# Kernel tuning notes

Hardware: AMD Instinct MI355X
Metric: run time of the kernel (lower is better)

The kernel has to match this reference:

```python
import jax, jax.numpy as jnp
import numpy as np

B, N, C, H = 4, 2048, 1024, 16
HD = C // H            # head dim = 64
HALF = HD // 2         # complex pairs per head = 32
VR = 32.0              # virtual_resolution
THETA = 10.0           # rope_theta


def _init_freqs():
    # mirrors init_3d_freqs_unified + per-axis replication with small noise
    rng = np.random.default_rng(0)
    idx = np.arange(HALF, dtype=np.float32)
    base = 1.0 / THETA ** (2.0 * idx / HD)                 # [HALF]
    angles = rng.uniform(0, 2 * np.pi, size=(H, 1)).astype(np.float32)
    per_head = base[None, :] * np.cos(angles)              # [H, HALF]
    freqs = np.repeat(per_head[None], 3, axis=0)           # [3, H, HALF]
    freqs = freqs + rng.normal(0, 0.01, freqs.shape).astype(np.float32)
    return jnp.asarray(freqs.reshape(3, H * HALF), dtype=jnp.float32)


def setup_inputs() -> dict:
    key = jax.random.key(0)
    ks = jax.random.split(key, 7)
    x = jax.random.normal(ks[0], (B, N, C), dtype=jnp.float32)
    t_x = jax.random.uniform(ks[1], (N,), dtype=jnp.float32)
    t_y = jax.random.uniform(ks[2], (N,), dtype=jnp.float32)
    t_z = jax.random.uniform(ks[3], (N,), dtype=jnp.float32)
    w_qkv = jax.random.normal(ks[4], (3 * C, C), dtype=jnp.float32) * (C ** -0.5)
    w_proj = jax.random.normal(ks[5], (C, C), dtype=jnp.float32) * (C ** -0.5)
    b_proj = jnp.zeros((C,), dtype=jnp.float32)
    freqs = _init_freqs()
    return {"x": x, "t_x": t_x, "t_y": t_y, "t_z": t_z,
            "w_qkv": w_qkv, "w_proj": w_proj, "b_proj": b_proj, "freqs": freqs}


def _normalize(t):
    # normalize_point_coords_3d with 'virtual_resolution'
    return (t - t.min()) / (t.max() - t.min() + 1e-8) * VR


def reference(x, t_x, t_y, t_z, w_qkv, w_proj, b_proj, freqs):
    # QKV projection (no bias)
    qkv = (x @ w_qkv.T).reshape(B, N, 3, H, HD).transpose(2, 0, 3, 1, 4)  # [3,B,H,N,HD]
    q, k, v = qkv[0], qkv[1], qkv[2]

    # mixed 3D RoPE angles: outer(t_axis, freqs[axis]) summed over axes
    tx, ty, tz = _normalize(t_x), _normalize(t_y), _normalize(t_z)
    ang = (tx[:, None] * freqs[0] + ty[:, None] * freqs[1] + tz[:, None] * freqs[2])  # [N, H*HALF]
    ang = ang.reshape(N, H, HALF).transpose(1, 0, 2)       # [H, N, HALF]
    cos, sin = jnp.cos(ang), jnp.sin(ang)

    def rotate(t):
        # complex multiply (a+ib)*(cos+isin) on even/odd pairs of last dim
        tr = t.reshape(B, H, N, HALF, 2)
        a, b = tr[..., 0], tr[..., 1]
        ra = a * cos - b * sin
        rb = a * sin + b * cos
        return jnp.stack([ra, rb], axis=-1).reshape(B, H, N, HD)

    q = rotate(q)
    k = rotate(k)

    scale = HD ** -0.5
    attn = jax.nn.softmax(jnp.einsum('bhnd,bhmd->bhnm', q * scale, k), axis=-1)
    out = jnp.einsum('bhnm,bhmd->bhnd', attn, v).transpose(0, 2, 1, 3).reshape(B, N, C)
    return out @ w_proj.T + b_proj
```

## Files before the change

kernel.cpp:

```cpp
#include <hip/hip_runtime.h>
#include <math.h>

#define BB 4
#define NN 2048
#define CC 1024
#define HH 16
#define HD 64
#define HALF 32
#define MM (BB*NN)
#define K3 (3*CC)
#define NF (HH*HALF)
#define NT (NN/64)

typedef __attribute__((ext_vector_type(8))) short bf16x8;
typedef __attribute__((ext_vector_type(4))) float f32x4;
typedef __attribute__((ext_vector_type(16))) float f32x16;
typedef __attribute__((ext_vector_type(4))) unsigned short u16x4;
typedef __attribute__((ext_vector_type(8))) unsigned short u16x8;
typedef __attribute__((ext_vector_type(4))) unsigned int u32x4;

#if __has_builtin(__builtin_amdgcn_exp2f)
#define EXP2(x) __builtin_amdgcn_exp2f(x)
#else
#define EXP2(x) exp2f(x)
#endif
#define AS1 __attribute__((address_space(1)))
#define AS3 __attribute__((address_space(3)))

__device__ __forceinline__ unsigned short f2bf(float f) {
    unsigned int u = __float_as_uint(f);
    unsigned int r = (u + 0x7FFFu + ((u >> 16) & 1u)) >> 16;
    return (unsigned short)r;
}

__global__ __launch_bounds__(256) void tnorm_kernel(const float* t_x, const float* t_y,
                                                    const float* t_z, float* tnorm) {
    int a = blockIdx.x;
    const float* t = (a == 0) ? t_x : ((a == 1) ? t_y : t_z);
    __shared__ float smn[256], smx[256];
    float mn = 1e30f, mx = -1e30f;
    for (int i = threadIdx.x; i < NN; i += 256) {
        float v = t[i];
        mn = fminf(mn, v);
        mx = fmaxf(mx, v);
    }
    smn[threadIdx.x] = mn; smx[threadIdx.x] = mx;
    __syncthreads();
    for (int s = 128; s > 0; s >>= 1) {
        if (threadIdx.x < s) {
            smn[threadIdx.x] = fminf(smn[threadIdx.x], smn[threadIdx.x + s]);
            smx[threadIdx.x] = fmaxf(smx[threadIdx.x], smx[threadIdx.x + s]);
        }
        __syncthreads();
    }
    float lo = smn[0];
    float sc = 32.0f / (smx[0] - lo + 1e-8f);
    for (int i = threadIdx.x; i < NN; i += 256)
        tnorm[a * NN + i] = (t[i] - lo) * sc;
}

__global__ __launch_bounds__(512) void angle_kernel(const float* freqs, const float* tnorm,
                                                    float* cosT, float* sinT) {
    int n = blockIdx.x;
    int hf = threadIdx.x;
    float ang = tnorm[n] * freqs[hf]
              + tnorm[NN + n] * freqs[NF + hf]
              + tnorm[2 * NN + n] * freqs[2 * NF + hf];
    cosT[(size_t)n * NF + hf] = cosf(ang);
    sinT[(size_t)n * NF + hf] = sinf(ang);
}

__global__ __launch_bounds__(256) void cvt_kernel(const float* __restrict__ src,
                                                  unsigned short* __restrict__ dst, int n) {
    int i = (blockIdx.x * 256 + threadIdx.x) * 8;
    if (i < n) {
        float4 a = *(const float4*)(src + i);
        float4 b = *(const float4*)(src + i + 4);
        u16x8 o;
        o[0] = f2bf(a.x); o[1] = f2bf(a.y); o[2] = f2bf(a.z); o[3] = f2bf(a.w);
        o[4] = f2bf(b.x); o[5] = f2bf(b.y); o[6] = f2bf(b.z); o[7] = f2bf(b.w);
        *(u16x8*)(dst + i) = o;
    }
}

__global__ __launch_bounds__(256) void qkv_gemm_kernel(const unsigned short* __restrict__ A,
                                                       const unsigned short* __restrict__ Bw,
                                                       const float* __restrict__ cosT,
                                                       const float* __restrict__ sinT,
                                                       unsigned short* __restrict__ qb,
                                                       unsigned short* __restrict__ kb,
                                                       unsigned short* __restrict__ vbT) {
    __shared__ unsigned short Asl[128 * 64];
    __shared__ unsigned short Bsl[128 * 64];
    const int tid = threadIdx.x;
    const int wv = tid >> 6, l = tid & 63;
    const int wm = wv >> 1, wn = wv & 1;
    const int lg = l >> 4, l15 = l & 15;
    const int m0 = blockIdx.x * 128, n0 = blockIdx.y * 128;

    f32x4 acc[4][4];
#pragma unroll
    for (int i = 0; i < 4; i++)
#pragma unroll
        for (int j = 0; j < 4; j++) acc[i][j] = f32x4{0.f, 0.f, 0.f, 0.f};

    for (int kt = 0; kt < CC; kt += 64) {
        __syncthreads();
#pragma unroll
        for (int i = 0; i < 4; i++) {
            int c = (wv * 4 + i) * 64 + l;
            int r = c >> 3, kc = c & 7;
            int sc = kt + ((kc ^ (r & 7)) * 8);
            __builtin_amdgcn_global_load_lds(
                (AS1 void*)(A + (size_t)(m0 + r) * CC + sc),
                (AS3 void*)(&Asl[(wv * 4 + i) * 512]), 16, 0, 0);
            __builtin_amdgcn_global_load_lds(
                (AS1 void*)(Bw + (size_t)(n0 + r) * CC + sc),
                (AS3 void*)(&Bsl[(wv * 4 + i) * 512]), 16, 0, 0);
        }
        __syncthreads();
#pragma unroll
        for (int kc = 0; kc < 2; kc++) {
            bf16x8 af[4], bfr[4];
#pragma unroll
            for (int mi = 0; mi < 4; mi++) {
                int r = wm * 64 + mi * 16 + l15;
                af[mi] = *(const bf16x8*)(&Asl[r * 64 + (((kc * 4 + lg) ^ (r & 7)) * 8)]);
            }
#pragma unroll
            for (int nj = 0; nj < 4; nj++) {
                int r = wn * 64 + nj * 16 + l15;
                bfr[nj] = *(const bf16x8*)(&Bsl[r * 64 + (((kc * 4 + lg) ^ (r & 7)) * 8)]);
            }
#pragma unroll
            for (int mi = 0; mi < 4; mi++)
#pragma unroll
                for (int nj = 0; nj < 4; nj++)
                    acc[mi][nj] = __builtin_amdgcn_mfma_f32_16x16x32_bf16(af[mi], bfr[nj], acc[mi][nj], 0, 0, 0);
        }
    }
    const int b_ = m0 >> 11;
    const int nrow0 = (m0 & (NN - 1));
#pragma unroll
    for (int nj = 0; nj < 4; nj++) {
        int oc = n0 + wn * 64 + nj * 16 + l15;
        int s = oc >> 10;
        int rr = oc & 1023;
        int h = rr >> 6;
        int d = rr & 63;
        int f = d >> 1;
#pragma unroll
        for (int mi = 0; mi < 4; mi++) {
            f32x4 v = acc[mi][nj];
            if (s == 2) {
                u16x4 vv;
#pragma unroll
                for (int reg = 0; reg < 4; reg++) vv[reg] = f2bf(v[reg]);
                int nb = nrow0 + wm * 64 + mi * 16 + lg * 4;
                *(u16x4*)(vbT + ((size_t)((b_ * HH + h) * HD + d)) * NN + nb) = vv;
            } else {
#pragma unroll
                for (int reg = 0; reg < 4; reg++) {
                    int m = m0 + wm * 64 + mi * 16 + lg * 4 + reg;
                    int n = m & (NN - 1);
                    float val = v[reg];
                    float partner = __shfl_xor(val, 1);
                    size_t base = (((size_t)(b_ * HH + h)) * NN + n) * HD + d;
                    float cs = cosT[(size_t)n * NF + h * HALF + f];
                    float sn = sinT[(size_t)n * NF + h * HALF + f];
                    float res = ((d & 1) == 0) ? (val * cs - partner * sn)
                                               : (val * cs + partner * sn);
                    if (s == 0) res *= 0.18033688011112043f;
                    (s == 0 ? qb : kb)[base] = f2bf(res);
                }
            }
        }
    }
}

template<int BUF>
__device__ __forceinline__ void attn_iter(
    unsigned short* LB, bool do_stage, int wv, int l31,
    const unsigned short*& kn0, const unsigned short*& kn1,
    const unsigned short*& vn0, const unsigned short*& vn1,
    const int (&so)[4], const bf16x8 (&qfA)[4], const bf16x8 (&qfB)[4],
    const f32x16& Z, const bf16x8& ones,
    f32x16& OA0, f32x16& OA1, f32x16& OB0, f32x16& OB1,
    f32x16& SsA, f32x16& SsB) {
    if (do_stage) {
        const int nb = (BUF ^ 1) * 4096;
        __builtin_amdgcn_global_load_lds((AS1 void*)kn0, (AS3 void*)(&LB[nb + (wv * 2 + 0) * 512]), 16, 0, 0);
        __builtin_amdgcn_global_load_lds((AS1 void*)kn1, (AS3 void*)(&LB[nb + (wv * 2 + 1) * 512]), 16, 0, 0);
        __builtin_amdgcn_global_load_lds((AS1 void*)vn0, (AS3 void*)(&LB[8192 + nb + (wv * 2 + 0) * 512]), 16, 0, 0);
        __builtin_amdgcn_global_load_lds((AS1 void*)vn1, (AS3 void*)(&LB[8192 + nb + (wv * 2 + 1) * 512]), 16, 0, 0);
        kn0 += 4096; kn1 += 4096; vn0 += 64; vn1 += 64;
    }
    f32x16 sA0, sA1, sB0, sB1;
    __builtin_amdgcn_s_setprio(1);
    {
        bf16x8 a0 = *(const bf16x8*)(LB + BUF * 4096 + l31 * 64 + so[0]);
        bf16x8 a1 = *(const bf16x8*)(LB + BUF * 4096 + (32 + l31) * 64 + so[0]);
        sA0 = __builtin_amdgcn_mfma_f32_32x32x16_bf16(a0, qfA[0], Z, 0, 0, 0);
        sA1 = __builtin_amdgcn_mfma_f32_32x32x16_bf16(a1, qfA[0], Z, 0, 0, 0);
        sB0 = __builtin_amdgcn_mfma_f32_32x32x16_bf16(a0, qfB[0], Z, 0, 0, 0);
        sB1 = __builtin_amdgcn_mfma_f32_32x32x16_bf16(a1, qfB[0], Z, 0, 0, 0);
    }
#pragma unroll
    for (int dc = 1; dc < 4; dc++) {
        bf16x8 a0 = *(const bf16x8*)(LB + BUF * 4096 + l31 * 64 + so[dc]);
        bf16x8 a1 = *(const bf16x8*)(LB + BUF * 4096 + (32 + l31) * 64 + so[dc]);
        sA0 = __builtin_amdgcn_mfma_f32_32x32x16_bf16(a0, qfA[dc], sA0, 0, 0, 0);
        sA1 = __builtin_amdgcn_mfma_f32_32x32x16_bf16(a1, qfA[dc], sA1, 0, 0, 0);
        sB0 = __builtin_amdgcn_mfma_f32_32x32x16_bf16(a0, qfB[dc], sB0, 0, 0, 0);
        sB1 = __builtin_amdgcn_mfma_f32_32x32x16_bf16(a1, qfB[dc], sB1, 0, 0, 0);
    }
    __builtin_amdgcn_s_setprio(0);
#pragma unroll
    for (int r = 0; r < 16; r++) {
        sA0[r] = EXP2(sA0[r]); sA1[r] = EXP2(sA1[r]);
        sB0[r] = EXP2(sB0[r]); sB1[r] = EXP2(sB1[r]);
    }
#pragma unroll
    for (int r = 0; r < 8; r++) {
        unsigned u0, u1, u2, u3;
        asm("v_cvt_pk_bf16_f32 %0, %1, %2" : "=v"(u0) : "v"(sA0[2 * r]), "v"(sA0[2 * r + 1]));
        asm("v_cvt_pk_bf16_f32 %0, %1, %2" : "=v"(u1) : "v"(sA1[2 * r]), "v"(sA1[2 * r + 1]));
        asm("v_cvt_pk_bf16_f32 %0, %1, %2" : "=v"(u2) : "v"(sB0[2 * r]), "v"(sB0[2 * r + 1]));
        asm("v_cvt_pk_bf16_f32 %0, %1, %2" : "=v"(u3) : "v"(sB1[2 * r]), "v"(sB1[2 * r + 1]));
        sA0[2 * r] = __uint_as_float(u0);
        sA1[2 * r] = __uint_as_float(u1);
        sB0[2 * r] = __uint_as_float(u2);
        sB1[2 * r] = __uint_as_float(u3);
    }
    __builtin_amdgcn_s_setprio(1);
#pragma unroll
    for (int kc = 0; kc < 4; kc++) {
        const int bs = (kc & 1) * 8;
        bf16x8 pfA, pfB;
        {
            float e0 = (kc < 2) ? sA0[bs + 0] : sA1[bs + 0];
            float e4 = (kc < 2) ? sA0[bs + 4] : sA1[bs + 4];
            float e2 = (kc < 2) ? sA0[bs + 2] : sA1[bs + 2];
            float e6 = (kc < 2) ? sA0[bs + 6] : sA1[bs + 6];
            auto uA = __builtin_amdgcn_permlane32_swap(__float_as_uint(e0), __float_as_uint(e4), false, false);
            auto uB = __builtin_amdgcn_permlane32_swap(__float_as_uint(e2), __float_as_uint(e6), false, false);
            u32x4 t; t.x = uA[0]; t.y = uB[0]; t.z = uA[1]; t.w = uB[1];
            pfA = __builtin_bit_cast(bf16x8, t);
        }
        {
            float e0 = (kc < 2) ? sB0[bs + 0] : sB1[bs + 0];
            float e4 = (kc < 2) ? sB0[bs + 4] : sB1[bs + 4];
            float e2 = (kc < 2) ? sB0[bs + 2] : sB1[bs + 2];
            float e6 = (kc < 2) ? sB0[bs + 6] : sB1[bs + 6];
            auto uA = __builtin_amdgcn_permlane32_swap(__float_as_uint(e0), __float_as_uint(e4), false, false);
            auto uB = __builtin_amdgcn_permlane32_swap(__float_as_uint(e2), __float_as_uint(e6), false, false);
            u32x4 t; t.x = uA[0]; t.y = uB[0]; t.z = uA[1]; t.w = uB[1];
            pfB = __builtin_bit_cast(bf16x8, t);
        }
        bf16x8 va  = *(const bf16x8*)(LB + 8192 + BUF * 4096 + l31 * 64 + so[kc]);
        bf16x8 vb2 = *(const bf16x8*)(LB + 8192 + BUF * 4096 + (32 + l31) * 64 + so[kc]);
        OA0 = __builtin_amdgcn_mfma_f32_32x32x16_bf16(va,  pfA, OA0, 0, 0, 0);
        OA1 = __builtin_amdgcn_mfma_f32_32x32x16_bf16(vb2, pfA, OA1, 0, 0, 0);
        OB0 = __builtin_amdgcn_mfma_f32_32x32x16_bf16(va,  pfB, OB0, 0, 0, 0);
        OB1 = __builtin_amdgcn_mfma_f32_32x32x16_bf16(vb2, pfB, OB1, 0, 0, 0);
        SsA = __builtin_amdgcn_mfma_f32_32x32x16_bf16(ones, pfA, SsA, 0, 0, 0);
        SsB = __builtin_amdgcn_mfma_f32_32x32x16_bf16(ones, pfB, SsB, 0, 0, 0);
    }
    __builtin_amdgcn_s_setprio(0);
    __syncthreads();
}

__global__ __launch_bounds__(256, 2) void attn_mfma_kernel(const unsigned short* __restrict__ qbp,
                                                           const unsigned short* __restrict__ kbp,
                                                           const unsigned short* __restrict__ vtp,
                                                           unsigned short* __restrict__ aout) {
    __shared__ unsigned short LB[4 * 4096];
    const int tid = threadIdx.x;
    const int wv = tid >> 6;
    const int l = tid & 63;
    const int l31 = l & 31, hi = l >> 5;

    const int wg = blockIdx.x;
    const int Lidx = (wg & 7) * 64 + (wg >> 3);
    const int bh = Lidx >> 3;
    const int q0 = (Lidx & 7) * 256;

    const unsigned short* qp = qbp + (size_t)bh * (NN * HD);
    const unsigned short* kp = kbp + (size_t)bh * (NN * HD);
    const unsigned short* vp = vtp + (size_t)bh * (NN * HD);

    const int r0 = (wv * 2 + 0) * 8 + (l >> 3);
    const int r1 = (wv * 2 + 1) * 8 + (l >> 3);
    const int c0 = ((l & 7) ^ (r0 & 7)) * 8;
    const int c1 = ((l & 7) ^ (r1 & 7)) * 8;
    const unsigned short* kn0 = kp + r0 * HD + c0;
    const unsigned short* kn1 = kp + r1 * HD + c1;
    const unsigned short* vn0 = vp + (size_t)r0 * NN + c0;
    const unsigned short* vn1 = vp + (size_t)r1 * NN + c1;

    __builtin_amdgcn_global_load_lds((AS1 void*)kn0, (AS3 void*)(&LB[(wv * 2 + 0) * 512]), 16, 0, 0);
    __builtin_amdgcn_global_load_lds((AS1 void*)kn1, (AS3 void*)(&LB[(wv * 2 + 1) * 512]), 16, 0, 0);
    __builtin_amdgcn_global_load_lds((AS1 void*)vn0, (AS3 void*)(&LB[8192 + (wv * 2 + 0) * 512]), 16, 0, 0);
    __builtin_amdgcn_global_load_lds((AS1 void*)vn1, (AS3 void*)(&LB[8192 + (wv * 2 + 1) * 512]), 16, 0, 0);
    kn0 += 4096; kn1 += 4096; vn0 += 64; vn1 += 64;

    const unsigned short* qr = qp + (size_t)(q0 + wv * 64 + l31) * HD;
    bf16x8 qfA[4], qfB[4];
#pragma unroll
    for (int dc = 0; dc < 4; dc++) {
        qfA[dc] = *(const bf16x8*)(qr + dc * 16 + hi * 8);
        qfB[dc] = *(const bf16x8*)(qr + 32 * HD + dc * 16 + hi * 8);
    }

    int so[4];
#pragma unroll
    for (int i = 0; i < 4; i++) so[i] = ((2 * i + hi) ^ (l31 & 7)) * 8;

    f32x16 Z;
#pragma unroll
    for (int r = 0; r < 16; r++) Z[r] = 0.0f;
    f32x16 OA0 = Z, OA1 = Z, OB0 = Z, OB1 = Z, SsA = Z, SsB = Z;
    bf16x8 ones;
#pragma unroll
    for (int j = 0; j < 8; j++) ones[j] = (short)0x3F80;

    __syncthreads();

    for (int ktb = 0; ktb < NT; ktb += 2) {
        attn_iter<0>(LB, true, wv, l31, kn0, kn1, vn0, vn1, so, qfA, qfB,
                     Z, ones, OA0, OA1, OB0, OB1, SsA, SsB);
        attn_iter<1>(LB, ktb + 2 < NT, wv, l31, kn0, kn1, vn0, vn1, so, qfA, qfB,
                     Z, ones, OA0, OA1, OB0, OB1, SsA, SsB);
    }

    const int b_ = bh >> 4, hh = bh & 15;
    const float invA = 1.0f / SsA[0], invB = 1.0f / SsB[0];
    const size_t mrowA = (size_t)(b_ * NN + q0 + wv * 64 + l31) * CC + hh * HD;
    const size_t mrowB = mrowA + (size_t)32 * CC;
#pragma unroll
    for (int rq = 0; rq < 4; rq++) {
        u16x4 a0, a1, b0, b1;
#pragma unroll
        for (int j = 0; j < 4; j++) {
            a0[j] = f2bf(OA0[rq * 4 + j] * invA);
            a1[j] = f2bf(OA1[rq * 4 + j] * invA);
            b0[j] = f2bf(OB0[rq * 4 + j] * invB);
            b1[j] = f2bf(OB1[rq * 4 + j] * invB);
        }
        *(u16x4*)(aout + mrowA + rq * 8 + hi * 4) = a0;
        *(u16x4*)(aout + mrowA + 32 + rq * 8 + hi * 4) = a1;
        *(u16x4*)(aout + mrowB + rq * 8 + hi * 4) = b0;
        *(u16x4*)(aout + mrowB + 32 + rq * 8 + hi * 4) = b1;
    }
}

__global__ __launch_bounds__(256) void proj_gemm_kernel(const unsigned short* __restrict__ A,
                                                        const unsigned short* __restrict__ Bw,
                                                        const float* __restrict__ bp,
                                                        float* __restrict__ out) {
    __shared__ unsigned short Asl[128 * 64];
    __shared__ unsigned short Bsl[128 * 64];
    const int tid = threadIdx.x;
    const int wv = tid >> 6, l = tid & 63;
    const int wm = wv >> 1, wn = wv & 1;
    const int lg = l >> 4, l15 = l & 15;
    const int m0 = blockIdx.x * 128, n0 = blockIdx.y * 128;

    f32x4 acc[4][4];
#pragma unroll
    for (int i = 0; i < 4; i++)
#pragma unroll
        for (int j = 0; j < 4; j++) acc[i][j] = f32x4{0.f, 0.f, 0.f, 0.f};

    for (int kt = 0; kt < CC; kt += 64) {
        __syncthreads();
#pragma unroll
        for (int i = 0; i < 4; i++) {
            int c = (wv * 4 + i) * 64 + l;
            int r = c >> 3, kc = c & 7;
            int sc = kt + ((kc ^ (r & 7)) * 8);
            __builtin_amdgcn_global_load_lds(
                (AS1 void*)(A + (size_t)(m0 + r) * CC + sc),
                (AS3 void*)(&Asl[(wv * 4 + i) * 512]), 16, 0, 0);
            __builtin_amdgcn_global_load_lds(
                (AS1 void*)(Bw + (size_t)(n0 + r) * CC + sc),
                (AS3 void*)(&Bsl[(wv * 4 + i) * 512]), 16, 0, 0);
        }
        __syncthreads();
#pragma unroll
        for (int kc = 0; kc < 2; kc++) {
            bf16x8 af[4], bfr[4];
#pragma unroll
            for (int mi = 0; mi < 4; mi++) {
                int r = wm * 64 + mi * 16 + l15;
                af[mi] = *(const bf16x8*)(&Asl[r * 64 + (((kc * 4 + lg) ^ (r & 7)) * 8)]);
            }
#pragma unroll
            for (int nj = 0; nj < 4; nj++) {
                int r = wn * 64 + nj * 16 + l15;
                bfr[nj] = *(const bf16x8*)(&Bsl[r * 64 + (((kc * 4 + lg) ^ (r & 7)) * 8)]);
            }
#pragma unroll
            for (int mi = 0; mi < 4; mi++)
#pragma unroll
                for (int nj = 0; nj < 4; nj++)
                    acc[mi][nj] = __builtin_amdgcn_mfma_f32_16x16x32_bf16(af[mi], bfr[nj], acc[mi][nj], 0, 0, 0);
        }
    }
    float bias[4];
#pragma unroll
    for (int nj = 0; nj < 4; nj++) bias[nj] = bp[n0 + wn * 64 + nj * 16 + l15];
#pragma unroll
    for (int mi = 0; mi < 4; mi++)
#pragma unroll
        for (int nj = 0; nj < 4; nj++) {
            int oc = n0 + wn * 64 + nj * 16 + l15;
#pragma unroll
            for (int reg = 0; reg < 4; reg++) {
                int m = m0 + wm * 64 + mi * 16 + lg * 4 + reg;
                out[(size_t)m * CC + oc] = acc[mi][nj][reg] + bias[nj];
            }
        }
}

extern "C" void kernel_launch(void* const* d_in, const int* in_sizes, int n_in,
                              void* d_out, int out_size, void* d_ws, size_t ws_size,
                              hipStream_t stream) {
    const float* x      = (const float*)d_in[0];
    const float* t_x    = (const float*)d_in[1];
    const float* t_y    = (const float*)d_in[2];
    const float* t_z    = (const float*)d_in[3];
    const float* w_qkv  = (const float*)d_in[4];
    const float* w_proj = (const float*)d_in[5];
    const float* b_proj = (const float*)d_in[6];
    const float* freqs  = (const float*)d_in[7];
    float* out = (float*)d_out;

    unsigned short* xb     = (unsigned short*)d_ws;
    unsigned short* wqkvb  = xb + (size_t)MM * CC;
    unsigned short* wprojb = wqkvb + (size_t)K3 * CC;
    unsigned short* qbuf   = wprojb + (size_t)CC * CC;
    unsigned short* kbuf   = qbuf + (size_t)BB * HH * NN * HD;
    unsigned short* vbT    = kbuf + (size_t)BB * HH * NN * HD;
    unsigned short* attnb  = vbT + (size_t)BB * HH * NN * HD;
    float* cosT  = (float*)(attnb + (size_t)MM * CC);
    float* sinT  = cosT + (size_t)NN * NF;
    float* tnorm = sinT + (size_t)NN * NF;

    tnorm_kernel<<<3, 256, 0, stream>>>(t_x, t_y, t_z, tnorm);
    angle_kernel<<<NN, 512, 0, stream>>>(freqs, tnorm, cosT, sinT);
    cvt_kernel<<<(MM * CC) / 2048, 256, 0, stream>>>(x, xb, MM * CC);
    cvt_kernel<<<(K3 * CC) / 2048, 256, 0, stream>>>(w_qkv, wqkvb, K3 * CC);
    cvt_kernel<<<(CC * CC) / 2048, 256, 0, stream>>>(w_proj, wprojb, CC * CC);
    qkv_gemm_kernel<<<dim3(MM / 128, K3 / 128), 256, 0, stream>>>(xb, wqkvb, cosT, sinT,
                                                                  qbuf, kbuf, vbT);
    attn_mfma_kernel<<<512, 256, 0, stream>>>(qbuf, kbuf, vbT, attnb);
    proj_gemm_kernel<<<dim3(MM / 128, CC / 128), 256, 0, stream>>>(attnb, wprojb, b_proj, out);
}
```

Measured before the change: 210.4 us.

## Switch attention to single-wave workgroups with 32-key tiles and no barriers

Restructures the attention kernel so each 64-thread workgroup holds one wave that owns 64 query rows, launching 2048 blocks instead of 512 four-wave blocks. K and V tiles shrink to 32 keys and are double-buffered in an 8192-element LDS buffer, with a new rotated-XOR swizzle for the staged layout. Block-wide __syncthreads is replaced by explicit s_waitcnt on vmcnt and lgkmcnt, so only the wave's own ordering is enforced. The intent is to remove barrier stalls and give the scheduler more independent waves, at the cost of each wave loading its own K/V with no sharing across waves and of smaller MFMA batches per iteration.

```diff
diff --git a/kernel.cpp b/kernel.cpp
--- a/kernel.cpp
+++ b/kernel.cpp
@@ -10,7 +10,8 @@
 #define MM (BB*NN)
 #define K3 (3*CC)
 #define NF (HH*HALF)
-#define NT (NN/64)
+#define TK 32
+#define NT2 (NN/TK)
 
 typedef __attribute__((ext_vector_type(8))) short bf16x8;
 typedef __attribute__((ext_vector_type(4))) float f32x4;
@@ -179,142 +180,143 @@
 }
 
 template<int BUF>
-__device__ __forceinline__ void attn_iter(
-    unsigned short* LB, bool do_stage, int wv, int l31,
-    const unsigned short*& kn0, const unsigned short*& kn1,
-    const unsigned short*& vn0, const unsigned short*& vn1,
-    const int (&so)[4], const bf16x8 (&qfA)[4], const bf16x8 (&qfB)[4],
+__device__ __forceinline__ void attn1w_iter(
+    unsigned short* LB,
+    const unsigned short* ks, const unsigned short* vs,
+    const int (&kso)[4], const int (&vso)[4],
+    const int (&kfo)[4], const int (&vfo)[4],
+    const bf16x8 (&qfA)[4], const bf16x8 (&qfB)[4],
     const f32x16& Z, const bf16x8& ones,
     f32x16& OA0, f32x16& OA1, f32x16& OB0, f32x16& OB1,
     f32x16& SsA, f32x16& SsB) {
-    if (do_stage) {
-        const int nb = (BUF ^ 1) * 4096;
-        __builtin_amdgcn_global_load_lds((AS1 void*)kn0, (AS3 void*)(&LB[nb + (wv * 2 + 0) * 512]), 16, 0, 0);
-        __builtin_amdgcn_global_load_lds((AS1 void*)kn1, (AS3 void*)(&LB[nb + (wv * 2 + 1) * 512]), 16, 0, 0);
-        __builtin_amdgcn_global_load_lds((AS1 void*)vn0, (AS3 void*)(&LB[8192 + nb + (wv * 2 + 0) * 512]), 16, 0, 0);
-        __builtin_amdgcn_global_load_lds((AS1 void*)vn1, (AS3 void*)(&LB[8192 + nb + (wv * 2 + 1) * 512]), 16, 0, 0);
-        kn0 += 4096; kn1 += 4096; vn0 += 64; vn1 += 64;
-    }
-    f32x16 sA0, sA1, sB0, sB1;
+    asm volatile("s_waitcnt lgkmcnt(0)" ::: "memory");
+    __builtin_amdgcn_sched_barrier(0);
+    const int nb = (BUF ^ 1) * 4096;
+#pragma unroll
+    for (int g = 0; g < 4; g++)
+        __builtin_amdgcn_global_load_lds((AS1 void*)(ks + kso[g]),
+                                         (AS3 void*)(&LB[nb + g * 512]), 16, 0, 0);
+#pragma unroll
+    for (int g = 0; g < 4; g++)
+        __builtin_amdgcn_global_load_lds((AS1 void*)(vs + vso[g]),
+                                         (AS3 void*)(&LB[nb + 2048 + g * 512]), 16, 0, 0);
+    __builtin_amdgcn_sched_barrier(0);
+    asm volatile("s_waitcnt vmcnt(8)" ::: "memory");
+    __builtin_amdgcn_sched_barrier(0);
+
+    const char* base = (const char*)LB + BUF * 8192;
+    f32x16 sA, sB;
     __builtin_amdgcn_s_setprio(1);
     {
-        bf16x8 a0 = *(const bf16x8*)(LB + BUF * 4096 + l31 * 64 + so[0]);
-        bf16x8 a1 = *(const bf16x8*)(LB + BUF * 4096 + (32 + l31) * 64 + so[0]);
-        sA0 = __builtin_amdgcn_mfma_f32_32x32x16_bf16(a0, qfA[0], Z, 0, 0, 0);
-        sA1 = __builtin_amdgcn_mfma_f32_32x32x16_bf16(a1, qfA[0], Z, 0, 0, 0);
-        sB0 = __builtin_amdgcn_mfma_f32_32x32x16_bf16(a0, qfB[0], Z, 0, 0, 0);
-        sB1 = __builtin_amdgcn_mfma_f32_32x32x16_bf16(a1, qfB[0], Z, 0, 0, 0);
+        bf16x8 a = *(const bf16x8*)(base + kfo[0]);
+        sA = __builtin_amdgcn_mfma_f32_32x32x16_bf16(a, qfA[0], Z, 0, 0, 0);
+        sB = __builtin_amdgcn_mfma_f32_32x32x16_bf16(a, qfB[0], Z, 0, 0, 0);
     }
 #pragma unroll
     for (int dc = 1; dc < 4; dc++) {
-        bf16x8 a0 = *(const bf16x8*)(LB + BUF * 4096 + l31 * 64 + so[dc]);
-        bf16x8 a1 = *(const bf16x8*)(LB + BUF * 4096 + (32 + l31) * 64 + so[dc]);
-        sA0 = __builtin_amdgcn_mfma_f32_32x32x16_bf16(a0, qfA[dc], sA0, 0, 0, 0);
-        sA1 = __builtin_amdgcn_mfma_f32_32x32x16_bf16(a1, qfA[dc], sA1, 0, 0, 0);
-        sB0 = __builtin_amdgcn_mfma_f32_32x32x16_bf16(a0, qfB[dc], sB0, 0, 0, 0);
-        sB1 = __builtin_amdgcn_mfma_f32_32x32x16_bf16(a1, qfB[dc], sB1, 0, 0, 0);
+        bf16x8 a = *(const bf16x8*)(base + kfo[dc]);
+        sA = __builtin_amdgcn_mfma_f32_32x32x16_bf16(a, qfA[dc], sA, 0, 0, 0);
+        sB = __builtin_amdgcn_mfma_f32_32x32x16_bf16(a, qfB[dc], sB, 0, 0, 0);
     }
     __builtin_amdgcn_s_setprio(0);
 #pragma unroll
-    for (int r = 0; r < 16; r++) {
-        sA0[r] = EXP2(sA0[r]); sA1[r] = EXP2(sA1[r]);
-        sB0[r] = EXP2(sB0[r]); sB1[r] = EXP2(sB1[r]);
-    }
+    for (int r = 0; r < 16; r++) { sA[r] = EXP2(sA[r]); sB[r] = EXP2(sB[r]); }
 #pragma unroll
     for (int r = 0; r < 8; r++) {
-        unsigned u0, u1, u2, u3;
-        asm("v_cvt_pk_bf16_f32 %0, %1, %2" : "=v"(u0) : "v"(sA0[2 * r]), "v"(sA0[2 * r + 1]));
-        asm("v_cvt_pk_bf16_f32 %0, %1, %2" : "=v"(u1) : "v"(sA1[2 * r]), "v"(sA1[2 * r + 1]));
-        asm("v_cvt_pk_bf16_f32 %0, %1, %2" : "=v"(u2) : "v"(sB0[2 * r]), "v"(sB0[2 * r + 1]));
-        asm("v_cvt_pk_bf16_f32 %0, %1, %2" : "=v"(u3) : "v"(sB1[2 * r]), "v"(sB1[2 * r + 1]));
-        sA0[2 * r] = __uint_as_float(u0);
-        sA1[2 * r] = __uint_as_float(u1);
-        sB0[2 * r] = __uint_as_float(u2);
-        sB1[2 * r] = __uint_as_float(u3);
+        unsigned u0, u1;
+        asm("v_cvt_pk_bf16_f32 %0, %1, %2" : "=v"(u0) : "v"(sA[2 * r]), "v"(sA[2 * r + 1]));
+        asm("v_cvt_pk_bf16_f32 %0, %1, %2" : "=v"(u1) : "v"(sB[2 * r]), "v"(sB[2 * r + 1]));
+        sA[2 * r] = __uint_as_float(u0);
+        sB[2 * r] = __uint_as_float(u1);
     }
     __builtin_amdgcn_s_setprio(1);
 #pragma unroll
-    for (int kc = 0; kc < 4; kc++) {
-        const int bs = (kc & 1) * 8;
+    for (int kc = 0; kc < 2; kc++) {
+        const int bs = kc * 8;
         bf16x8 pfA, pfB;
         {
-            float e0 = (kc < 2) ? sA0[bs + 0] : sA1[bs + 0];
-            float e4 = (kc < 2) ? sA0[bs + 4] : sA1[bs + 4];
-            float e2 = (kc < 2) ? sA0[bs + 2] : sA1[bs + 2];
-            float e6 = (kc < 2) ? sA0[bs + 6] : sA1[bs + 6];
-            auto uA = __builtin_amdgcn_permlane32_swap(__float_as_uint(e0), __float_as_uint(e4), false, false);
-            auto uB = __builtin_amdgcn_permlane32_swap(__float_as_uint(e2), __float_as_uint(e6), false, false);
+            auto uA = __builtin_amdgcn_permlane32_swap(__float_as_uint(sA[bs + 0]), __float_as_uint(sA[bs + 4]), false, false);
+            auto uB = __builtin_amdgcn_permlane32_swap(__float_as_uint(sA[bs + 2]), __float_as_uint(sA[bs + 6]), false, false);
             u32x4 t; t.x = uA[0]; t.y = uB[0]; t.z = uA[1]; t.w = uB[1];
             pfA = __builtin_bit_cast(bf16x8, t);
         }
         {
-            float e0 = (kc < 2) ? sB0[bs + 0] : sB1[bs + 0];
-            float e4 = (kc < 2) ? sB0[bs + 4] : sB1[bs + 4];
-            float e2 = (kc < 2) ? sB0[bs + 2] : sB1[bs + 2];
-            float e6 = (kc < 2) ? sB0[bs + 6] : sB1[bs + 6];
-            auto uA = __builtin_amdgcn_permlane32_swap(__float_as_uint(e0), __float_as_uint(e4), false, false);
-            auto uB = __builtin_amdgcn_permlane32_swap(__float_as_uint(e2), __float_as_uint(e6), false, false);
+            auto uA = __builtin_amdgcn_permlane32_swap(__float_as_uint(sB[bs + 0]), __float_as_uint(sB[bs + 4]), false, false);
+            auto uB = __builtin_amdgcn_permlane32_swap(__float_as_uint(sB[bs + 2]), __float_as_uint(sB[bs + 6]), false, false);
             u32x4 t; t.x = uA[0]; t.y = uB[0]; t.z = uA[1]; t.w = uB[1];
             pfB = __builtin_bit_cast(bf16x8, t);
         }
-        bf16x8 va  = *(const bf16x8*)(LB + 8192 + BUF * 4096 + l31 * 64 + so[kc]);
-        bf16x8 vb2 = *(const bf16x8*)(LB + 8192 + BUF * 4096 + (32 + l31) * 64 + so[kc]);
-        OA0 = __builtin_amdgcn_mfma_f32_32x32x16_bf16(va,  pfA, OA0, 0, 0, 0);
-        OA1 = __builtin_amdgcn_mfma_f32_32x32x16_bf16(vb2, pfA, OA1, 0, 0, 0);
-        OB0 = __builtin_amdgcn_mfma_f32_32x32x16_bf16(va,  pfB, OB0, 0, 0, 0);
-        OB1 = __builtin_amdgcn_mfma_f32_32x32x16_bf16(vb2, pfB, OB1, 0, 0, 0);
+        bf16x8 v0 = *(const bf16x8*)(base + vfo[kc]);
+        bf16x8 v1 = *(const bf16x8*)(base + vfo[2 + kc]);
+        OA0 = __builtin_amdgcn_mfma_f32_32x32x16_bf16(v0, pfA, OA0, 0, 0, 0);
+        OA1 = __builtin_amdgcn_mfma_f32_32x32x16_bf16(v1, pfA, OA1, 0, 0, 0);
+        OB0 = __builtin_amdgcn_mfma_f32_32x32x16_bf16(v0, pfB, OB0, 0, 0, 0);
+        OB1 = __builtin_amdgcn_mfma_f32_32x32x16_bf16(v1, pfB, OB1, 0, 0, 0);
         SsA = __builtin_amdgcn_mfma_f32_32x32x16_bf16(ones, pfA, SsA, 0, 0, 0);
         SsB = __builtin_amdgcn_mfma_f32_32x32x16_bf16(ones, pfB, SsB, 0, 0, 0);
     }
     __builtin_amdgcn_s_setprio(0);
-    __syncthreads();
-}
-
-__global__ __launch_bounds__(256, 2) void attn_mfma_kernel(const unsigned short* __restrict__ qbp,
-                                                           const unsigned short* __restrict__ kbp,
-                                                           const unsigned short* __restrict__ vtp,
-                                                           unsigned short* __restrict__ aout) {
-    __shared__ unsigned short LB[4 * 4096];
-    const int tid = threadIdx.x;
-    const int wv = tid >> 6;
-    const int l = tid & 63;
+}
+
+__global__ __launch_bounds__(64, 2) void attn_mfma_kernel(const unsigned short* __restrict__ qbp,
+                                                          const unsigned short* __restrict__ kbp,
+                                                          const unsigned short* __restrict__ vtp,
+                                                          unsigned short* __restrict__ aout) {
+    __shared__ unsigned short LB[8192];
+    const int l = threadIdx.x;
     const int l31 = l & 31, hi = l >> 5;
 
     const int wg = blockIdx.x;
-    const int Lidx = (wg & 7) * 64 + (wg >> 3);
-    const int bh = Lidx >> 3;
-    const int q0 = (Lidx & 7) * 256;
+    const int Lidx = (wg & 7) * 256 + (wg >> 3);
+    const int bh = Lidx >> 5;
+    const int q0 = (Lidx & 31) * 64;
 
     const unsigned short* qp = qbp + (size_t)bh * (NN * HD);
     const unsigned short* kp = kbp + (size_t)bh * (NN * HD);
     const unsigned short* vp = vtp + (size_t)bh * (NN * HD);
 
-    const int r0 = (wv * 2 + 0) * 8 + (l >> 3);
-    const int r1 = (wv * 2 + 1) * 8 + (l >> 3);
-    const int c0 = ((l & 7) ^ (r0 & 7)) * 8;
-    const int c1 = ((l & 7) ^ (r1 & 7)) * 8;
-    const unsigned short* kn0 = kp + r0 * HD + c0;
-    const unsigned short* kn1 = kp + r1 * HD + c1;
-    const unsigned short* vn0 = vp + (size_t)r0 * NN + c0;
-    const unsigned short* vn1 = vp + (size_t)r1 * NN + c1;
-
-    __builtin_amdgcn_global_load_lds((AS1 void*)kn0, (AS3 void*)(&LB[(wv * 2 + 0) * 512]), 16, 0, 0);
-    __builtin_amdgcn_global_load_lds((AS1 void*)kn1, (AS3 void*)(&LB[(wv * 2 + 1) * 512]), 16, 0, 0);
-    __builtin_amdgcn_global_load_lds((AS1 void*)vn0, (AS3 void*)(&LB[8192 + (wv * 2 + 0) * 512]), 16, 0, 0);
-    __builtin_amdgcn_global_load_lds((AS1 void*)vn1, (AS3 void*)(&LB[8192 + (wv * 2 + 1) * 512]), 16, 0, 0);
-    kn0 += 4096; kn1 += 4096; vn0 += 64; vn1 += 64;
-
-    const unsigned short* qr = qp + (size_t)(q0 + wv * 64 + l31) * HD;
+    const int s7 = l & 7;
+    int kso[4], vso[4];
+#pragma unroll
+    for (int g = 0; g < 4; g++) {
+        int r = 8 * g + (l >> 3);
+        int c = ((s7 - (r >> 3)) & 7) ^ (r & 7);
+        kso[g] = r * HD + c * 8;
+        vso[g] = (r + (c >> 2) * 32) * NN + (c & 3) * 8;
+    }
+    int kfo[4], vfo[4];
+#pragma unroll
+    for (int dc = 0; dc < 4; dc++) {
+        int c = 2 * dc + hi;
+        int sl = ((c ^ (l31 & 7)) + (l31 >> 3)) & 7;
+        kfo[dc] = l31 * 128 + sl * 16;
+    }
+#pragma unroll
+    for (int idx = 0; idx < 4; idx++) {
+        int dt = idx >> 1, kc = idx & 1;
+        int c = dt * 4 + kc * 2 + hi;
+        int sl = ((c ^ (l31 & 7)) + (l31 >> 3)) & 7;
+        vfo[idx] = 4096 + l31 * 128 + sl * 16;
+    }
+
+#pragma unroll
+    for (int g = 0; g < 4; g++)
+        __builtin_amdgcn_global_load_lds((AS1 void*)(kp + kso[g]),
+                                         (AS3 void*)(&LB[g * 512]), 16, 0, 0);
+#pragma unroll
+    for (int g = 0; g < 4; g++)
+        __builtin_amdgcn_global_load_lds((AS1 void*)(vp + vso[g]),
+                                         (AS3 void*)(&LB[2048 + g * 512]), 16, 0, 0);
+    __builtin_amdgcn_sched_barrier(0);
+
+    const unsigned short* qr = qp + (size_t)(q0 + l31) * HD;
     bf16x8 qfA[4], qfB[4];
 #pragma unroll
     for (int dc = 0; dc < 4; dc++) {
         qfA[dc] = *(const bf16x8*)(qr + dc * 16 + hi * 8);
         qfB[dc] = *(const bf16x8*)(qr + 32 * HD + dc * 16 + hi * 8);
     }
-
-    int so[4];
-#pragma unroll
-    for (int i = 0; i < 4; i++) so[i] = ((2 * i + hi) ^ (l31 & 7)) * 8;
+    __builtin_amdgcn_sched_barrier(0);
 
     f32x16 Z;
 #pragma unroll
@@ -324,18 +326,21 @@
 #pragma unroll
     for (int j = 0; j < 8; j++) ones[j] = (short)0x3F80;
 
-    __syncthreads();
-
-    for (int ktb = 0; ktb < NT; ktb += 2) {
-        attn_iter<0>(LB, true, wv, l31, kn0, kn1, vn0, vn1, so, qfA, qfB,
-                     Z, ones, OA0, OA1, OB0, OB1, SsA, SsB);
-        attn_iter<1>(LB, ktb + 2 < NT, wv, l31, kn0, kn1, vn0, vn1, so, qfA, qfB,
-                     Z, ones, OA0, OA1, OB0, OB1, SsA, SsB);
+    const unsigned short* ks = kp + TK * HD;
+    const unsigned short* vs = vp + TK;
+#pragma unroll 1
+    for (int t = 0; t < NT2; t += 2) {
+        attn1w_iter<0>(LB, ks, vs, kso, vso, kfo, vfo, qfA, qfB, Z, ones,
+                       OA0, OA1, OB0, OB1, SsA, SsB);
+        if (t + 2 < NT2) { ks += TK * HD; vs += TK; }
+        attn1w_iter<1>(LB, ks, vs, kso, vso, kfo, vfo, qfA, qfB, Z, ones,
+                       OA0, OA1, OB0, OB1, SsA, SsB);
+        if (t + 3 < NT2) { ks += TK * HD; vs += TK; }
     }
 
     const int b_ = bh >> 4, hh = bh & 15;
     const float invA = 1.0f / SsA[0], invB = 1.0f / SsB[0];
-    const size_t mrowA = (size_t)(b_ * NN + q0 + wv * 64 + l31) * CC + hh * HD;
+    const size_t mrowA = (size_t)(b_ * NN + q0 + l31) * CC + hh * HD;
     const size_t mrowB = mrowA + (size_t)32 * CC;
 #pragma unroll
     for (int rq = 0; rq < 4; rq++) {
@@ -454,6 +459,6 @@
     cvt_kernel<<<(CC * CC) / 2048, 256, 0, stream>>>(w_proj, wprojb, CC * CC);
     qkv_gemm_kernel<<<dim3(MM / 128, K3 / 128), 256, 0, stream>>>(xb, wqkvb, cosT, sinT,
                                                                   qbuf, kbuf, vbT);
-    attn_mfma_kernel<<<512, 256, 0, stream>>>(qbuf, kbuf, vbT, attnb);
+    attn_mfma_kernel<<<2048, 64, 0, stream>>>(qbuf, kbuf, vbT, attnb);
     proj_gemm_kernel<<<dim3(MM / 128, CC / 128), 256, 0, stream>>>(attnb, wprojb, b_proj, out);
 }
```

After: 223.0 us. +6.0%, slower.
